# Kernel tuning notes

Hardware: AMD Instinct MI355X
Metric: run time of the kernel (lower is better)

The kernel has to match this reference:

```python
import jax, jax.numpy as jnp
import numpy as np

B, S, H = 2, 2048, 2048
E, K = 16, 4
I_MOE, I_SH = 1408, 5632


def setup_inputs() -> dict:
    key = jax.random.key(0)
    ks = jax.random.split(key, 9)
    def w(k, shape, fan_in):
        return jax.random.normal(k, shape, jnp.float32) * (fan_in ** -0.5)
    return {
        "hidden_states": jax.random.normal(ks[0], (B, S, H), jnp.float32),
        "router_w": w(ks[1], (E, H), H),           # router gate weight [E, H]
        "w_gate": w(ks[2], (E, H, I_MOE), H),       # stacked expert gate_proj
        "w_up": w(ks[3], (E, H, I_MOE), H),         # stacked expert up_proj
        "w_down": w(ks[4], (E, I_MOE, H), I_MOE),   # stacked expert down_proj
        "sh_gate": w(ks[5], (H, I_SH), H),          # shared expert gate_proj
        "sh_up": w(ks[6], (H, I_SH), H),            # shared expert up_proj
        "sh_down": w(ks[7], (I_SH, H), I_SH),       # shared expert down_proj
        "sh_gate_w": w(ks[8], (H, 1), H),           # shared_expert_gate (Linear H->1)
    }


def reference(hidden_states, router_w, w_gate, w_up, w_down,
              sh_gate, sh_up, sh_down, sh_gate_w):
    orig = hidden_states.shape
    h = hidden_states.reshape(-1, orig[-1])  # [N, H]
    N = h.shape[0]

    # --- router: softmax (fp32) -> top-k -> renormalise ---
    logits = h @ router_w.T                               # [N, E]
    probs = jax.nn.softmax(logits.astype(jnp.float32), axis=-1)
    top_vals, top_idx = jax.lax.top_k(probs, K)           # [N, K]
    top_vals = top_vals / jnp.maximum(top_vals.sum(-1, keepdims=True), 1e-9)
    top_vals = top_vals.astype(h.dtype)

    # combine weights: [N, E], gate value where routed, 0 elsewhere
    comb = jnp.zeros((N, E), h.dtype).at[jnp.arange(N)[:, None], top_idx].add(top_vals)

    # --- routed experts (dense-over-experts, masked combine == gather/scatter math) ---
    g = jnp.einsum('nh,ehi->eni', h, w_gate)              # [E, N, I]
    u = jnp.einsum('nh,ehi->eni', h, w_up)                # [E, N, I]
    y = jnp.einsum('eni,eih->enh', jax.nn.silu(g) * u, w_down)  # [E, N, H]
    routed = jnp.einsum('enh,ne->nh', y, comb)            # [N, H]

    # --- shared expert with sigmoid gate ---
    shared = (jax.nn.silu(h @ sh_gate) * (h @ sh_up)) @ sh_down  # [N, H]
    sg = jax.nn.sigmoid(h @ sh_gate_w)                    # [N, 1]

    return (routed + sg * shared).reshape(orig)
```

## Files before the change

kernel.cpp:

```cpp
#include <hip/hip_runtime.h>
#include <stdint.h>


#define N_TOK 4096
#define H_DIM 2048
#define E_NUM 16
#define TOPK  4
#define IMOE  1408
#define ISH   5632
#define SLOTS (N_TOK*TOPK)

#define MT 128
#define BK 64

typedef __attribute__((ext_vector_type(8))) short bf16x8;
typedef __attribute__((ext_vector_type(4))) float f32x4;

static __device__ inline unsigned short f2bf(float f) {
    union { float f; unsigned u; } v; v.f = f;
    unsigned r = v.u + 0x7fffu + ((v.u >> 16) & 1u);
    return (unsigned short)(r >> 16);
}

static __device__ inline void glds16(const unsigned short* g, unsigned short* l) {
    __builtin_amdgcn_global_load_lds(
        (const __attribute__((address_space(1))) void*)g,
        (__attribute__((address_space(3))) void*)l, 16, 0, 0);
}

static __device__ inline bool decode_tile(int bx, int by, int NX, int NYact,
                                          int& nt, int& mt) {
    int f = by * NX + bx;
    int NB = NX * NYact;
    if (f >= NB) return false;
    int q = NB >> 3, rr = NB & 7;
    int x = f & 7, s = f >> 3;
    int L = (x < rr ? x * (q + 1) : rr * (q + 1) + (x - rr) * q) + s;
    const int GM = 8;
    int G = GM * NX;
    int g = L / G, r2 = L - g * G;
    int gm = NYact - g * GM; if (gm > GM) gm = GM;
    nt = r2 / gm;
    mt = g * GM + (r2 - nt * gm);
    return true;
}

__global__ void cvt_h_kernel(const float* __restrict__ in, unsigned short* __restrict__ out, int n4) {
    int i = blockIdx.x * blockDim.x + threadIdx.x;
    if (i < n4) {
        float4 v = *(const float4*)(in + (size_t)i * 4);
        ushort4 o; o.x = f2bf(v.x); o.y = f2bf(v.y); o.z = f2bf(v.z); o.w = f2bf(v.w);
        *(ushort4*)(out + (size_t)i * 4) = o;
    }
}

__global__ void transpose_cvt_kernel(const float* __restrict__ in, unsigned short* __restrict__ out,
                                     int R, int C) {
    __shared__ float tile[32][33];
    const float* ip = in + (size_t)blockIdx.z * R * C;
    unsigned short* op = out + (size_t)blockIdx.z * R * C;
    int cb = blockIdx.x * 32, rb = blockIdx.y * 32;
    int tx = threadIdx.x, ty = threadIdx.y;
    for (int i = 0; i < 4; i++)
        tile[ty + i * 8][tx] = ip[(size_t)(rb + ty + i * 8) * C + cb + tx];
    __syncthreads();
    for (int i = 0; i < 4; i++)
        op[(size_t)(cb + ty + i * 8) * R + rb + tx] = f2bf(tile[tx][ty + i * 8]);
}

__global__ __launch_bounds__(256) void router_kernel(
    const float* __restrict__ h, const float* __restrict__ rw, const float* __restrict__ gw,
    int* __restrict__ topk_idx, float* __restrict__ topk_w,
    float* __restrict__ sg, int* __restrict__ counts) {
    int n = blockIdx.x;
    const float* hp = h + (size_t)n * H_DIM;
    int t = threadIdx.x;
    int e = t >> 4, part = t & 15;
    const float* rp = rw + (size_t)e * H_DIM;
    float acc = 0.f;
    for (int j = part; j < H_DIM; j += 16) acc += hp[j] * rp[j];
    for (int d = 8; d; d >>= 1) acc += __shfl_down(acc, d, 16);
    __shared__ float logits[E_NUM];
    if (part == 0) logits[e] = acc;
    float sacc = 0.f;
    for (int j = t; j < H_DIM; j += 256) sacc += hp[j] * gw[j];
    __shared__ float sred[256];
    sred[t] = sacc;
    __syncthreads();
    for (int d = 128; d; d >>= 1) { if (t < d) sred[t] += sred[t + d]; __syncthreads(); }
    if (t == 0) {
        float m = logits[0];
        for (int i = 1; i < E_NUM; i++) m = fmaxf(m, logits[i]);
        float p[E_NUM]; float s = 0.f;
        for (int i = 0; i < E_NUM; i++) { p[i] = expf(logits[i] - m); s += p[i]; }
        float invs = 1.f / s;
        for (int i = 0; i < E_NUM; i++) p[i] *= invs;
        int idx[TOPK]; float val[TOPK]; float vs = 0.f;
        for (int k = 0; k < TOPK; k++) {
            int bi = 0; float bv = -1.f;
            for (int i = 0; i < E_NUM; i++) if (p[i] > bv) { bv = p[i]; bi = i; }
            idx[k] = bi; val[k] = bv; vs += bv; p[bi] = -2.f;
        }
        float inv = 1.f / fmaxf(vs, 1e-9f);
        for (int k = 0; k < TOPK; k++) {
            topk_idx[n * TOPK + k] = idx[k];
            topk_w[n * TOPK + k] = val[k] * inv;
            atomicAdd(&counts[idx[k]], 1);
        }
        sg[n] = 1.f / (1.f + expf(-sred[0]));
    }
}

__global__ void scan_kernel(const int* __restrict__ counts, int* __restrict__ offsets,
                            int* __restrict__ cursor) {
    int s = 0;
    for (int e = 0; e < E_NUM; e++) { offsets[e] = s; cursor[e] = s; s += counts[e]; }
}

__global__ void bucketize_kernel(const int* __restrict__ topk_idx, const float* __restrict__ topk_w,
                                 int* __restrict__ cursor, int* __restrict__ slot_tok,
                                 float* __restrict__ slot_w) {
    int n = blockIdx.x * blockDim.x + threadIdx.x;
    if (n >= N_TOK) return;
    for (int k = 0; k < TOPK; k++) {
        int e = topk_idx[n * TOPK + k];
        int s = atomicAdd(&cursor[e], 1);
        slot_tok[s] = n;
        slot_w[s] = topk_w[n * TOPK + k];
    }
}

__global__ __launch_bounds__(256) void gather_kernel(const unsigned short* __restrict__ hbf,
                                                     const int* __restrict__ slot_tok,
                                                     unsigned short* __restrict__ A) {
    int s = blockIdx.x;
    int tok = slot_tok[s];
    const uint4* src = (const uint4*)(hbf + (size_t)tok * H_DIM);
    uint4* dst = (uint4*)(A + (size_t)s * H_DIM);
    dst[threadIdx.x] = src[threadIdx.x];
}

__global__ __launch_bounds__(256, 2) void gemm_dual_kernel(
    const unsigned short* __restrict__ A, const unsigned short* __restrict__ Bg,
    const unsigned short* __restrict__ Bu, unsigned short* __restrict__ act,
    const int* __restrict__ counts, const int* __restrict__ offsets,
    int K, int N, int fixedM) {
    int e = blockIdx.z;
    int c, off;
    if (counts) { c = counts[e]; off = offsets[e]; } else { c = fixedM; off = 0; }
    int NYact = (c + MT - 1) / MT;
    int nt, mt;
    if (!decode_tile(blockIdx.x, blockIdx.y, gridDim.x, NYact, nt, mt)) return;

    const unsigned short* Ab = A + (size_t)off * K;
    const unsigned short* Bgb = Bg + (size_t)e * (size_t)N * K;
    const unsigned short* Bub = Bu + (size_t)e * (size_t)N * K;
    unsigned short* actb = act + (size_t)off * N;

    __shared__ __align__(16) unsigned short As[MT * BK];
    __shared__ __align__(16) unsigned short Bgs[64 * BK];
    __shared__ __align__(16) unsigned short Bus[64 * BK];

    int t = threadIdx.x;
    int wave = t >> 6, lane = t & 63;
    int wm = wave >> 1, wn = wave & 1;
    int quad = lane >> 4, l16 = lane & 15;

    f32x4 accg[4][2], accu[4][2];
    for (int i = 0; i < 4; i++) for (int j = 0; j < 2; j++) { accg[i][j] = (f32x4)0.f; accu[i][j] = (f32x4)0.f; }

    int m0 = mt * MT, n0 = nt * 64;
    int rA[4], cA[4];
    for (int j = 0; j < 4; j++) { int s = t + 256 * j; rA[j] = s >> 3; cA[j] = (s & 7) ^ (rA[j] & 7); }
    int rB[2], cB[2];
    for (int j = 0; j < 2; j++) { int s = t + 256 * j; rB[j] = s >> 3; cB[j] = (s & 7) ^ (rB[j] & 7); }

    for (int kt = 0; kt < K; kt += BK) {
        __syncthreads();
        for (int j = 0; j < 4; j++)
            glds16(&Ab[(size_t)(m0 + rA[j]) * K + kt + cA[j] * 8], &As[(t + 256 * j) * 8]);
        for (int j = 0; j < 2; j++) {
            glds16(&Bgb[(size_t)(n0 + rB[j]) * K + kt + cB[j] * 8], &Bgs[(t + 256 * j) * 8]);
            glds16(&Bub[(size_t)(n0 + rB[j]) * K + kt + cB[j] * 8], &Bus[(t + 256 * j) * 8]);
        }
        __syncthreads();
#pragma unroll
        for (int ks = 0; ks < 2; ks++) {
            int lbase = (ks << 2) | quad;
            bf16x8 af[4], bgf[2], buf[2];
            for (int mi = 0; mi < 4; mi++) {
                int rowl = wm * 64 + mi * 16 + l16;
                af[mi] = *(const bf16x8*)&As[rowl * BK + ((lbase ^ (rowl & 7)) * 8)];
            }
            for (int ni = 0; ni < 2; ni++) {
                int rowl = wn * 32 + ni * 16 + l16;
                int co = (lbase ^ (rowl & 7)) * 8;
                bgf[ni] = *(const bf16x8*)&Bgs[rowl * BK + co];
                buf[ni] = *(const bf16x8*)&Bus[rowl * BK + co];
            }
            for (int mi = 0; mi < 4; mi++)
                for (int ni = 0; ni < 2; ni++) {
                    accg[mi][ni] = __builtin_amdgcn_mfma_f32_16x16x32_bf16(af[mi], bgf[ni], accg[mi][ni], 0, 0, 0);
                    accu[mi][ni] = __builtin_amdgcn_mfma_f32_16x16x32_bf16(af[mi], buf[ni], accu[mi][ni], 0, 0, 0);
                }
        }
    }
    for (int mi = 0; mi < 4; mi++) {
        for (int r = 0; r < 4; r++) {
            int rl = m0 + wm * 64 + mi * 16 + quad * 4 + r;
            if (rl < c) {
                size_t rowbase = (size_t)rl * N + n0 + wn * 32 + l16;
                for (int ni = 0; ni < 2; ni++) {
                    float g = accg[mi][ni][r];
                    float u = accu[mi][ni][r];
                    float a = (g / (1.f + __expf(-g))) * u;
                    actb[rowbase + ni * 16] = f2bf(a);
                }
            }
        }
    }
}

__global__ __launch_bounds__(256, 2) void gemm_down_kernel(
    const unsigned short* __restrict__ Aact, const unsigned short* __restrict__ Bd,
    float* __restrict__ out,
    const int* __restrict__ counts, const int* __restrict__ offsets,
    const int* __restrict__ slot_tok, const float* __restrict__ slot_w,
    const float* __restrict__ sg,
    int K, int N, int fixedM) {
    int e = blockIdx.z;
    bool routed = (counts != nullptr);
    int c, off;
    if (routed) { c = counts[e]; off = offsets[e]; } else { c = fixedM; off = 0; }
    int NYact = (c + MT - 1) / MT;
    int nt, mt;
    if (!decode_tile(blockIdx.x, blockIdx.y, gridDim.x, NYact, nt, mt)) return;

    const unsigned short* Ab = Aact + (size_t)off * K;
    const unsigned short* Bb = Bd + (size_t)e * (size_t)N * K;

    __shared__ __align__(16) unsigned short As[MT * BK];
    __shared__ __align__(16) unsigned short Bs[MT * BK];

    int t = threadIdx.x;
    int wave = t >> 6, lane = t & 63;
    int wm = wave >> 1, wn = wave & 1;
    int quad = lane >> 4, l16 = lane & 15;

    f32x4 acc[4][4];
    for (int i = 0; i < 4; i++) for (int j = 0; j < 4; j++) acc[i][j] = (f32x4)0.f;

    int m0 = mt * MT, n0 = nt * MT;
    int rA[4], cA[4];
    for (int j = 0; j < 4; j++) { int s = t + 256 * j; rA[j] = s >> 3; cA[j] = (s & 7) ^ (rA[j] & 7); }

    for (int kt = 0; kt < K; kt += BK) {
        __syncthreads();
        for (int j = 0; j < 4; j++) {
            glds16(&Ab[(size_t)(m0 + rA[j]) * K + kt + cA[j] * 8], &As[(t + 256 * j) * 8]);
            glds16(&Bb[(size_t)(n0 + rA[j]) * K + kt + cA[j] * 8], &Bs[(t + 256 * j) * 8]);
        }
        __syncthreads();
#pragma unroll
        for (int ks = 0; ks < 2; ks++) {
            int lbase = (ks << 2) | quad;
            bf16x8 af[4], bf[4];
            for (int mi = 0; mi < 4; mi++) {
                int rowl = wm * 64 + mi * 16 + l16;
                af[mi] = *(const bf16x8*)&As[rowl * BK + ((lbase ^ (rowl & 7)) * 8)];
            }
            for (int ni = 0; ni < 4; ni++) {
                int rowl = wn * 64 + ni * 16 + l16;
                bf[ni] = *(const bf16x8*)&Bs[rowl * BK + ((lbase ^ (rowl & 7)) * 8)];
            }
            for (int mi = 0; mi < 4; mi++)
                for (int ni = 0; ni < 4; ni++)
                    acc[mi][ni] = __builtin_amdgcn_mfma_f32_16x16x32_bf16(af[mi], bf[ni], acc[mi][ni], 0, 0, 0);
        }
    }
    for (int mi = 0; mi < 4; mi++) {
        for (int r = 0; r < 4; r++) {
            int rl = m0 + wm * 64 + mi * 16 + quad * 4 + r;
            if (rl < c) {
                int col = n0 + wn * 64 + l16;
                if (routed) {
                    int s = off + rl;
                    int tok = slot_tok[s];
                    float w = slot_w[s];
                    float* ob = out + (size_t)tok * N + col;
                    for (int ni = 0; ni < 4; ni++)
                        atomicAdd(ob + ni * 16, w * acc[mi][ni][r]);
                } else {
                    float w = sg[rl];
                    float* ob = out + (size_t)rl * N + col;
                    for (int ni = 0; ni < 4; ni++)
                        ob[ni * 16] += w * acc[mi][ni][r];
                }
            }
        }
    }
}

extern "C" void kernel_launch(void* const* d_in, const int* in_sizes, int n_in,
                              void* d_out, int out_size, void* d_ws, size_t ws_size,
                              hipStream_t stream) {
    const float* h   = (const float*)d_in[0];
    const float* rw  = (const float*)d_in[1];
    const float* wg  = (const float*)d_in[2];
    const float* wu  = (const float*)d_in[3];
    const float* wd  = (const float*)d_in[4];
    const float* shg = (const float*)d_in[5];
    const float* shu = (const float*)d_in[6];
    const float* shd = (const float*)d_in[7];
    const float* sgw = (const float*)d_in[8];
    float* out = (float*)d_out;

    char* ws = (char*)d_ws;
    size_t off = 0;
    auto alloc = [&](size_t b) { size_t o = off; off += (b + 255) & ~(size_t)255; return (void*)(ws + o); };

    int*   counts   = (int*)  alloc(E_NUM * 4);
    int*   offsets  = (int*)  alloc(E_NUM * 4);
    int*   cursor   = (int*)  alloc(E_NUM * 4);
    int*   topk_idx = (int*)  alloc((size_t)N_TOK * TOPK * 4);
    float* topk_w   = (float*)alloc((size_t)N_TOK * TOPK * 4);
    float* sg       = (float*)alloc((size_t)N_TOK * 4);
    int*   slot_tok = (int*)  alloc((size_t)SLOTS * 4);
    float* slot_w   = (float*)alloc((size_t)SLOTS * 4);
    unsigned short* h_bf  = (unsigned short*)alloc((size_t)N_TOK * H_DIM * 2);
    unsigned short* wgT   = (unsigned short*)alloc((size_t)E_NUM * IMOE * H_DIM * 2);
    unsigned short* wuT   = (unsigned short*)alloc((size_t)E_NUM * IMOE * H_DIM * 2);
    unsigned short* wdT   = (unsigned short*)alloc((size_t)E_NUM * H_DIM * IMOE * 2);
    unsigned short* shGT  = (unsigned short*)alloc((size_t)ISH * H_DIM * 2);
    unsigned short* shUT  = (unsigned short*)alloc((size_t)ISH * H_DIM * 2);
    unsigned short* shDT  = (unsigned short*)alloc((size_t)H_DIM * ISH * 2);
    unsigned short* Agath = (unsigned short*)alloc((size_t)(SLOTS + MT) * H_DIM * 2);
    unsigned short* actR  = (unsigned short*)alloc((size_t)(SLOTS + MT) * IMOE * 2);
    unsigned short* actS  = (unsigned short*)alloc((size_t)N_TOK * ISH * 2);
    (void)ws_size; (void)in_sizes; (void)n_in; (void)out_size;

    hipMemsetAsync(out, 0, (size_t)N_TOK * H_DIM * 4, stream);
    hipMemsetAsync(counts, 0, E_NUM * 4, stream);

    cvt_h_kernel<<<(N_TOK * H_DIM / 4 + 255) / 256, 256, 0, stream>>>(h, h_bf, N_TOK * H_DIM / 4);
    transpose_cvt_kernel<<<dim3(IMOE / 32, H_DIM / 32, E_NUM), dim3(32, 8), 0, stream>>>(wg, wgT, H_DIM, IMOE);
    transpose_cvt_kernel<<<dim3(IMOE / 32, H_DIM / 32, E_NUM), dim3(32, 8), 0, stream>>>(wu, wuT, H_DIM, IMOE);
    transpose_cvt_kernel<<<dim3(H_DIM / 32, IMOE / 32, E_NUM), dim3(32, 8), 0, stream>>>(wd, wdT, IMOE, H_DIM);
    transpose_cvt_kernel<<<dim3(ISH / 32, H_DIM / 32, 1), dim3(32, 8), 0, stream>>>(shg, shGT, H_DIM, ISH);
    transpose_cvt_kernel<<<dim3(ISH / 32, H_DIM / 32, 1), dim3(32, 8), 0, stream>>>(shu, shUT, H_DIM, ISH);
    transpose_cvt_kernel<<<dim3(H_DIM / 32, ISH / 32, 1), dim3(32, 8), 0, stream>>>(shd, shDT, ISH, H_DIM);

    router_kernel<<<N_TOK, 256, 0, stream>>>(h, rw, sgw, topk_idx, topk_w, sg, counts);
    scan_kernel<<<1, 1, 0, stream>>>(counts, offsets, cursor);
    bucketize_kernel<<<N_TOK / 256, 256, 0, stream>>>(topk_idx, topk_w, cursor, slot_tok, slot_w);
    gather_kernel<<<SLOTS, 256, 0, stream>>>(h_bf, slot_tok, Agath);

    gemm_dual_kernel<<<dim3(IMOE / 64, N_TOK / MT, E_NUM), 256, 0, stream>>>(
        Agath, wgT, wuT, actR, counts, offsets, H_DIM, IMOE, 0);
    gemm_dual_kernel<<<dim3(ISH / 64, N_TOK / MT, 1), 256, 0, stream>>>(
        h_bf, shGT, shUT, actS, nullptr, nullptr, H_DIM, ISH, N_TOK);
    gemm_down_kernel<<<dim3(H_DIM / MT, N_TOK / MT, E_NUM), 256, 0, stream>>>(
        actR, wdT, out, counts, offsets, slot_tok, slot_w, nullptr, IMOE, H_DIM, 0);
    gemm_down_kernel<<<dim3(H_DIM / MT, N_TOK / MT, 1), 256, 0, stream>>>(
        actS, shDT, out, nullptr, nullptr, nullptr, nullptr, sg, ISH, H_DIM, N_TOK);
}
```

Before: 1.651 ms.

## Restructure router to process 16 tokens per block with register accumulators

The router kernel now gives each block 16 tokens, one per group of 16 lanes. Every lane holds 17 accumulators (16 expert logits plus the shared gate) and reads hidden states and weights as float4. This removes the per-token shared-memory tree reduction and its barriers, and lets each hidden-state load be reused across all experts. The top-k selection now uses a bitmask instead of overwriting probabilities. The cost is higher register pressure and fewer blocks.

```diff
diff --git a/kernel.cpp b/kernel.cpp
--- a/kernel.cpp
+++ b/kernel.cpp
@@ -72,42 +72,60 @@
     const float* __restrict__ h, const float* __restrict__ rw, const float* __restrict__ gw,
     int* __restrict__ topk_idx, float* __restrict__ topk_w,
     float* __restrict__ sg, int* __restrict__ counts) {
-    int n = blockIdx.x;
+    int t = threadIdx.x;
+    int wv = t >> 6, lane = t & 63;
+    int tokw = lane >> 4, part = lane & 15;
+    int n = blockIdx.x * 16 + wv * 4 + tokw;
     const float* hp = h + (size_t)n * H_DIM;
-    int t = threadIdx.x;
-    int e = t >> 4, part = t & 15;
-    const float* rp = rw + (size_t)e * H_DIM;
-    float acc = 0.f;
-    for (int j = part; j < H_DIM; j += 16) acc += hp[j] * rp[j];
-    for (int d = 8; d; d >>= 1) acc += __shfl_down(acc, d, 16);
-    __shared__ float logits[E_NUM];
-    if (part == 0) logits[e] = acc;
-    float sacc = 0.f;
-    for (int j = t; j < H_DIM; j += 256) sacc += hp[j] * gw[j];
-    __shared__ float sred[256];
-    sred[t] = sacc;
-    __syncthreads();
-    for (int d = 128; d; d >>= 1) { if (t < d) sred[t] += sred[t + d]; __syncthreads(); }
-    if (t == 0) {
-        float m = logits[0];
-        for (int i = 1; i < E_NUM; i++) m = fmaxf(m, logits[i]);
+
+    float acc[17];
+#pragma unroll
+    for (int e = 0; e < 17; e++) acc[e] = 0.f;
+
+    for (int i = 0; i < 32; i++) {
+        int j = i * 64 + part * 4;
+        float4 hv = *(const float4*)(hp + j);
+#pragma unroll
+        for (int e = 0; e < E_NUM; e++) {
+            float4 w4 = *(const float4*)(rw + (size_t)e * H_DIM + j);
+            acc[e] += hv.x * w4.x + hv.y * w4.y + hv.z * w4.z + hv.w * w4.w;
+        }
+        float4 g4 = *(const float4*)(gw + j);
+        acc[16] += hv.x * g4.x + hv.y * g4.y + hv.z * g4.z + hv.w * g4.w;
+    }
+#pragma unroll
+    for (int d = 8; d; d >>= 1)
+#pragma unroll
+        for (int e = 0; e < 17; e++)
+            acc[e] += __shfl_down(acc[e], d, 16);
+
+    if (part == 0) {
+        float m = acc[0];
+#pragma unroll
+        for (int i = 1; i < E_NUM; i++) m = fmaxf(m, acc[i]);
         float p[E_NUM]; float s = 0.f;
-        for (int i = 0; i < E_NUM; i++) { p[i] = expf(logits[i] - m); s += p[i]; }
+#pragma unroll
+        for (int i = 0; i < E_NUM; i++) { p[i] = expf(acc[i] - m); s += p[i]; }
         float invs = 1.f / s;
+#pragma unroll
         for (int i = 0; i < E_NUM; i++) p[i] *= invs;
-        int idx[TOPK]; float val[TOPK]; float vs = 0.f;
+        int idx[TOPK]; float val[TOPK]; float vs = 0.f; unsigned used = 0;
+#pragma unroll
         for (int k = 0; k < TOPK; k++) {
             int bi = 0; float bv = -1.f;
-            for (int i = 0; i < E_NUM; i++) if (p[i] > bv) { bv = p[i]; bi = i; }
-            idx[k] = bi; val[k] = bv; vs += bv; p[bi] = -2.f;
+#pragma unroll
+            for (int i = 0; i < E_NUM; i++)
+                if (!((used >> i) & 1u) && p[i] > bv) { bv = p[i]; bi = i; }
+            idx[k] = bi; val[k] = bv; vs += bv; used |= (1u << bi);
         }
         float inv = 1.f / fmaxf(vs, 1e-9f);
+#pragma unroll
         for (int k = 0; k < TOPK; k++) {
             topk_idx[n * TOPK + k] = idx[k];
             topk_w[n * TOPK + k] = val[k] * inv;
             atomicAdd(&counts[idx[k]], 1);
         }
-        sg[n] = 1.f / (1.f + expf(-sred[0]));
+        sg[n] = 1.f / (1.f + expf(-acc[16]));
     }
 }
 
@@ -350,7 +368,7 @@
     transpose_cvt_kernel<<<dim3(ISH / 32, H_DIM / 32, 1), dim3(32, 8), 0, stream>>>(shu, shUT, H_DIM, ISH);
     transpose_cvt_kernel<<<dim3(H_DIM / 32, ISH / 32, 1), dim3(32, 8), 0, stream>>>(shd, shDT, ISH, H_DIM);
 
-    router_kernel<<<N_TOK, 256, 0, stream>>>(h, rw, sgw, topk_idx, topk_w, sg, counts);
+    router_kernel<<<N_TOK / 16, 256, 0, stream>>>(h, rw, sgw, topk_idx, topk_w, sg, counts);
     scan_kernel<<<1, 1, 0, stream>>>(counts, offsets, cursor);
     bucketize_kernel<<<N_TOK / 256, 256, 0, stream>>>(topk_idx, topk_w, cursor, slot_tok, slot_w);
     gather_kernel<<<SLOTS, 256, 0, stream>>>(h_bf, slot_tok, Agath);
```

After: 1.495 ms. 9.4% less time.
